# Kernel optimization log

Measured on AMD Instinct MI355X. Metric: run time of the kernel, lower is better.

Reference implementation:

```python
import jax, jax.numpy as jnp
import numpy as np

N_NODES = 50000
N_EDGES = 500000
IN_CH = 128
OUT_CH = 256


def setup_inputs() -> dict:
    key = jax.random.key(0)
    k1, k2, k3, k4, k5 = jax.random.split(key, 5)
    x = jax.random.normal(k1, (N_NODES, IN_CH), dtype=jnp.float32)
    edge_index = jax.random.randint(k2, (2, N_EDGES), 0, N_NODES, dtype=jnp.int64)
    edge_weight = jax.random.normal(k3, (N_EDGES,), dtype=jnp.float32)
    # GCNConv linear weight (xavier-uniform) and bias (zeros in torch init; use randn for generality)
    limit = float(np.sqrt(6.0 / (IN_CH + OUT_CH)))
    W = jax.random.uniform(k4, (IN_CH, OUT_CH), minval=-limit, maxval=limit, dtype=jnp.float32)
    b = jnp.zeros((OUT_CH,), dtype=jnp.float32)
    return {"x": x, "W": W, "b": b, "edge_index": edge_index, "edge_weight": edge_weight}


def reference(x, W, b, edge_index, edge_weight):
    N = x.shape[0]
    # GCN wrapper applies sigmoid to edge weights before GCNConv
    ew = jax.nn.sigmoid(edge_weight)
    # gcn_norm: add self-loops with weight 1
    loop = jnp.arange(N, dtype=edge_index.dtype)
    row = jnp.concatenate([edge_index[0], loop])  # source nodes
    col = jnp.concatenate([edge_index[1], loop])  # target nodes
    w = jnp.concatenate([ew, jnp.ones((N,), dtype=x.dtype)])
    # degree on target index, symmetric normalization
    deg = jax.ops.segment_sum(w, col, num_segments=N)
    dinv = jnp.where(deg > 0, jax.lax.rsqrt(deg), jnp.zeros_like(deg))
    norm = dinv[row] * w * dinv[col]  # [E+N]
    # linear transform first (GCNConv: lin has no bias; bias added after aggregation)
    h = x @ W  # [N, OUT_CH]
    msg = h[row] * norm[:, None]  # gather + scale  [E+N, OUT_CH]
    out = jax.ops.segment_sum(msg, col, num_segments=N) + b
    return out
```

## Files before the change

kernel.cpp:

```cpp
#include <hip/hip_runtime.h>
#include <hip/hip_bf16.h>
#include <math.h>

#define NN 50000
#define NE 500000
#define IC 128
#define OC 256
#define NPAD 50176
#define NB 196
#define NEB 1954
#define CAP 64

typedef short bf16x8 __attribute__((ext_vector_type(8)));
typedef float f32x4 __attribute__((ext_vector_type(4)));

static __device__ inline unsigned short f2b(float f) {
    __hip_bfloat16 h = __float2bfloat16(f);
    return *reinterpret_cast<unsigned short*>(&h);
}
static __device__ inline float b2f(short u) {
    unsigned v = ((unsigned)(unsigned short)u) << 16;
    return __int_as_float(v);
}

__global__ void k_init(unsigned long long* __restrict__ deg64) {
    int i = blockIdx.x * 256 + threadIdx.x;
    deg64[i] = (unsigned long long)(1u << 24);
}

__global__ void k_pass1(const int* __restrict__ row,
                        const int* __restrict__ col,
                        const float* __restrict__ ew,
                        unsigned long long* __restrict__ deg64,
                        int2* __restrict__ epack,
                        const float* __restrict__ x,
                        unsigned short* __restrict__ xb,
                        const float* __restrict__ W,
                        unsigned short* __restrict__ WT) {
    int g = blockIdx.x * 256 + threadIdx.x;
    if (g < NE) {
        int c = col[g];
        float w = 1.0f / (1.0f + expf(-ew[g]));
        unsigned long long pack = (1ull << 32) | (unsigned long long)(unsigned)(w * 16777216.0f);
        unsigned long long old = atomicAdd(&deg64[c], pack);
        int ord = (int)(old >> 32);
        if (ord < CAP) {
            int2 p;
            p.x = row[g];
            p.y = __float_as_int(w);
            epack[(size_t)c * CAP + ord] = p;
        }
    }
    const int NX = NN * (IC / 4);
    for (int i = g; i < NX; i += NEB * 256) {
        float4 v = ((const float4*)x)[i];
        ushort4 o;
        o.x = f2b(v.x); o.y = f2b(v.y); o.z = f2b(v.z); o.w = f2b(v.w);
        ((ushort4*)xb)[i] = o;
    }
    if (g < IC * OC) {
        int k = g >> 8;
        int n = g & 255;
        WT[n * IC + k] = f2b(W[g]);
    }
}

__global__ void k_dinv(const unsigned long long* __restrict__ deg64,
                       float* __restrict__ dinv) {
    int i = blockIdx.x * 256 + threadIdx.x;
    unsigned long long v = deg64[i];
    float deg = (float)(unsigned)v * (1.0f / 16777216.0f);
    dinv[i] = rsqrtf(deg);
}

__global__ __launch_bounds__(256) void k_gather_gemm(
        const unsigned short* __restrict__ xb,
        const unsigned long long* __restrict__ deg64,
        const int2* __restrict__ epack,
        const float* __restrict__ dinv,
        const unsigned short* __restrict__ WT,
        const float* __restrict__ bias,
        float* __restrict__ out) {
    __shared__ __align__(16) unsigned short a[16][136];

    const int base = blockIdx.x * 16;
    const int g = threadIdx.x >> 4;
    const int l16 = threadIdx.x & 15;
    const int n = base + g;
    const bf16x8* xv = (const bf16x8*)xb;

    float di = dinv[n];
    unsigned long long dv = deg64[n];
    int cnt = (int)(dv >> 32);
    if (cnt > CAP) cnt = CAP;

    bf16x8 xs = xv[(size_t)n * 16 + l16];
    float acc[8];
    float s2 = di * di;
    #pragma unroll
    for (int c = 0; c < 8; ++c) acc[c] = b2f(xs[c]) * s2;

    const int2* ep = epack + (size_t)n * CAP;
    int e = 0;
    for (; e + 2 <= cnt; e += 2) {
        int2 p0 = ep[e];
        int2 p1 = ep[e + 1];
        float w0 = __int_as_float(p0.y) * dinv[p0.x] * di;
        float w1 = __int_as_float(p1.y) * dinv[p1.x] * di;
        bf16x8 v0 = xv[(size_t)p0.x * 16 + l16];
        bf16x8 v1 = xv[(size_t)p1.x * 16 + l16];
        #pragma unroll
        for (int c = 0; c < 8; ++c) acc[c] += b2f(v0[c]) * w0;
        #pragma unroll
        for (int c = 0; c < 8; ++c) acc[c] += b2f(v1[c]) * w1;
    }
    if (e < cnt) {
        int2 p = ep[e];
        float w = __int_as_float(p.y) * dinv[p.x] * di;
        bf16x8 v = xv[(size_t)p.x * 16 + l16];
        #pragma unroll
        for (int c = 0; c < 8; ++c) acc[c] += b2f(v[c]) * w;
    }

    bf16x8 o;
    #pragma unroll
    for (int c = 0; c < 8; ++c) o[c] = (short)f2b(acc[c]);
    *(bf16x8*)(&a[g][l16 * 8]) = o;

    __syncthreads();

    const int w = threadIdx.x >> 6;
    const int lane = threadIdx.x & 63;
    const int n0 = w * 64;
    const int lm = lane & 15;
    const int lk = (lane >> 4) * 8;

    f32x4 acc4[4] = {};
    #pragma unroll
    for (int ks = 0; ks < 4; ++ks) {
        const int k0 = ks * 32 + lk;
        bf16x8 wf[4];
        #pragma unroll
        for (int j = 0; j < 4; ++j)
            wf[j] = *(const bf16x8*)(WT + (size_t)(n0 + j * 16 + lm) * IC + k0);
        bf16x8 af = *(const bf16x8*)(&a[lm][k0]);
        #pragma unroll
        for (int j = 0; j < 4; ++j)
            acc4[j] = __builtin_amdgcn_mfma_f32_16x16x32_bf16(wf[j], af, acc4[j], 0, 0, 0);
    }

    const int mcol = lane & 15;
    const int nb4 = (lane >> 4) * 4;
    const int m = base + mcol;
    #pragma unroll
    for (int j = 0; j < 4; ++j) {
        int nn = n0 + j * 16 + nb4;
        float4 bv = *(const float4*)&bias[nn];
        float4 ov;
        ov.x = acc4[j][0] + bv.x;
        ov.y = acc4[j][1] + bv.y;
        ov.z = acc4[j][2] + bv.z;
        ov.w = acc4[j][3] + bv.w;
        *(float4*)(out + (size_t)m * OC + nn) = ov;
    }
}

extern "C" void kernel_launch(void* const* d_in, const int* in_sizes, int n_in,
                              void* d_out, int out_size, void* d_ws, size_t ws_size,
                              hipStream_t stream) {
    const float* x  = (const float*)d_in[0];
    const float* W  = (const float*)d_in[1];
    const float* b  = (const float*)d_in[2];
    const int*   ei = (const int*)d_in[3];
    const float* ew = (const float*)d_in[4];
    const int* row = ei;
    const int* col = ei + NE;
    float* out = (float*)d_out;

    char* w0 = (char*)d_ws;
    unsigned long long* deg64 = (unsigned long long*)w0;  w0 += NPAD * 8;
    float* dinv  = (float*)w0;                   w0 += NPAD * 4;
    int2*  epack = (int2*)w0;                    w0 += (size_t)NN * CAP * 8;
    unsigned short* WT   = (unsigned short*)w0;  w0 += IC * OC * 2;
    unsigned short* xb   = (unsigned short*)w0;

    k_init       <<<NB, 256, 0, stream>>>(deg64);
    k_pass1      <<<NEB, 256, 0, stream>>>(row, col, ew, deg64, epack, x, xb, W, WT);
    k_dinv       <<<NB, 256, 0, stream>>>(deg64, dinv);
    k_gather_gemm<<<NN / 16, 256, 0, stream>>>(xb, deg64, epack, dinv, WT, b, out);
}
```

Baseline: 175.6 us.

## Pack edges into 32-bit words and process 32 nodes per gather-GEMM block

Each edge entry shrinks from 8 to 4 bytes by storing a 16-bit source index with an fp16 sigmoid weight. The gather-GEMM block now handles 32 nodes, with 8 lanes per node each loading two bf16x8 chunks. The next edge pair is prefetched, and each loaded W fragment feeds two MFMA row tiles, halving W loads per node. This lowers edge-list traffic and W reloads, at the cost of reduced edge-weight precision, a 16-bit node-index limit, and a prefetch read past each list that relies on padding.

```diff
diff --git a/kernel.cpp b/kernel.cpp
--- a/kernel.cpp
+++ b/kernel.cpp
@@ -1,5 +1,6 @@
 #include <hip/hip_runtime.h>
 #include <hip/hip_bf16.h>
+#include <hip/hip_fp16.h>
 #include <math.h>
 
 #define NN 50000
@@ -22,6 +23,10 @@
     unsigned v = ((unsigned)(unsigned short)u) << 16;
     return __int_as_float(v);
 }
+static __device__ inline float h2f(unsigned short h) {
+    __half v = __ushort_as_half(h);
+    return __half2float(v);
+}
 
 __global__ void k_init(unsigned long long* __restrict__ deg64) {
     int i = blockIdx.x * 256 + threadIdx.x;
@@ -32,7 +37,7 @@
                         const int* __restrict__ col,
                         const float* __restrict__ ew,
                         unsigned long long* __restrict__ deg64,
-                        int2* __restrict__ epack,
+                        unsigned* __restrict__ epack,
                         const float* __restrict__ x,
                         unsigned short* __restrict__ xb,
                         const float* __restrict__ W,
@@ -45,9 +50,8 @@
         unsigned long long old = atomicAdd(&deg64[c], pack);
         int ord = (int)(old >> 32);
         if (ord < CAP) {
-            int2 p;
-            p.x = row[g];
-            p.y = __float_as_int(w);
+            unsigned short wh = __half_as_ushort(__float2half_rn(w));
+            unsigned p = ((unsigned)wh << 16) | (unsigned)row[g];
             epack[(size_t)c * CAP + ord] = p;
         }
     }
@@ -76,56 +80,70 @@
 __global__ __launch_bounds__(256) void k_gather_gemm(
         const unsigned short* __restrict__ xb,
         const unsigned long long* __restrict__ deg64,
-        const int2* __restrict__ epack,
+        const unsigned* __restrict__ epack,
         const float* __restrict__ dinv,
         const unsigned short* __restrict__ WT,
         const float* __restrict__ bias,
         float* __restrict__ out) {
-    __shared__ __align__(16) unsigned short a[16][136];
-
-    const int base = blockIdx.x * 16;
-    const int g = threadIdx.x >> 4;
-    const int l16 = threadIdx.x & 15;
+    __shared__ __align__(16) unsigned short a[32][136];
+
+    const int base = blockIdx.x * 32;
+    const int g = threadIdx.x >> 3;
+    const int l8 = threadIdx.x & 7;
     const int n = base + g;
     const bf16x8* xv = (const bf16x8*)xb;
 
-    float di = dinv[n];
-    unsigned long long dv = deg64[n];
-    int cnt = (int)(dv >> 32);
-    if (cnt > CAP) cnt = CAP;
-
-    bf16x8 xs = xv[(size_t)n * 16 + l16];
-    float acc[8];
-    float s2 = di * di;
+    float acc[16];
+    if (n < NN) {
+        float di = dinv[n];
+        unsigned long long dv = deg64[n];
+        int cnt = (int)(dv >> 32);
+        if (cnt > CAP) cnt = CAP;
+        float s2 = di * di;
+
+        bf16x8 xs0 = xv[(size_t)n * 16 + l8];
+        bf16x8 xs1 = xv[(size_t)n * 16 + 8 + l8];
+        #pragma unroll
+        for (int c = 0; c < 8; ++c) { acc[c] = b2f(xs0[c]) * s2; acc[8 + c] = b2f(xs1[c]) * s2; }
+
+        const unsigned* ep = epack + (size_t)n * CAP;
+        int e = 0;
+        uint2 pq = *(const uint2*)ep;
+        for (; e + 2 <= cnt; e += 2) {
+            unsigned p0 = pq.x, p1 = pq.y;
+            pq = *(const uint2*)(ep + e + 2);
+            int r0 = (int)(p0 & 0xFFFFu);
+            int r1 = (int)(p1 & 0xFFFFu);
+            float w0 = h2f((unsigned short)(p0 >> 16)) * dinv[r0] * di;
+            float w1 = h2f((unsigned short)(p1 >> 16)) * dinv[r1] * di;
+            bf16x8 v00 = xv[(size_t)r0 * 16 + l8];
+            bf16x8 v01 = xv[(size_t)r0 * 16 + 8 + l8];
+            bf16x8 v10 = xv[(size_t)r1 * 16 + l8];
+            bf16x8 v11 = xv[(size_t)r1 * 16 + 8 + l8];
+            #pragma unroll
+            for (int c = 0; c < 8; ++c) { acc[c] += b2f(v00[c]) * w0; acc[8 + c] += b2f(v01[c]) * w0; }
+            #pragma unroll
+            for (int c = 0; c < 8; ++c) { acc[c] += b2f(v10[c]) * w1; acc[8 + c] += b2f(v11[c]) * w1; }
+        }
+        if (e < cnt) {
+            unsigned p = pq.x;
+            int r = (int)(p & 0xFFFFu);
+            float w = h2f((unsigned short)(p >> 16)) * dinv[r] * di;
+            bf16x8 v0 = xv[(size_t)r * 16 + l8];
+            bf16x8 v1 = xv[(size_t)r * 16 + 8 + l8];
+            #pragma unroll
+            for (int c = 0; c < 8; ++c) { acc[c] += b2f(v0[c]) * w; acc[8 + c] += b2f(v1[c]) * w; }
+        }
+    } else {
+        #pragma unroll
+        for (int c = 0; c < 16; ++c) acc[c] = 0.0f;
+    }
+
+    bf16x8 o0, o1;
     #pragma unroll
-    for (int c = 0; c < 8; ++c) acc[c] = b2f(xs[c]) * s2;
-
-    const int2* ep = epack + (size_t)n * CAP;
-    int e = 0;
-    for (; e + 2 <= cnt; e += 2) {
-        int2 p0 = ep[e];
-        int2 p1 = ep[e + 1];
-        float w0 = __int_as_float(p0.y) * dinv[p0.x] * di;
-        float w1 = __int_as_float(p1.y) * dinv[p1.x] * di;
-        bf16x8 v0 = xv[(size_t)p0.x * 16 + l16];
-        bf16x8 v1 = xv[(size_t)p1.x * 16 + l16];
-        #pragma unroll
-        for (int c = 0; c < 8; ++c) acc[c] += b2f(v0[c]) * w0;
-        #pragma unroll
-        for (int c = 0; c < 8; ++c) acc[c] += b2f(v1[c]) * w1;
-    }
-    if (e < cnt) {
-        int2 p = ep[e];
-        float w = __int_as_float(p.y) * dinv[p.x] * di;
-        bf16x8 v = xv[(size_t)p.x * 16 + l16];
-        #pragma unroll
-        for (int c = 0; c < 8; ++c) acc[c] += b2f(v[c]) * w;
-    }
-
-    bf16x8 o;
-    #pragma unroll
-    for (int c = 0; c < 8; ++c) o[c] = (short)f2b(acc[c]);
-    *(bf16x8*)(&a[g][l16 * 8]) = o;
+    for (int c = 0; c < 8; ++c) { o0[c] = (short)f2b(acc[c]); o1[c] = (short)f2b(acc[8 + c]); }
+    *(bf16x8*)(&a[g][l8 * 8]) = o0;
+    *(bf16x8*)(&a[g][64 + l8 * 8]) = o1;
 
     __syncthreads();
 
@@ -135,33 +153,42 @@
     const int lm = lane & 15;
     const int lk = (lane >> 4) * 8;
 
-    f32x4 acc4[4] = {};
+    f32x4 acc4[2][4] = {};
     #pragma unroll
     for (int ks = 0; ks < 4; ++ks) {
         const int k0 = ks * 32 + lk;
-        bf16x8 wf[4];
+        bf16x8 wf[4], af[2];
         #pragma unroll
         for (int j = 0; j < 4; ++j)
             wf[j] = *(const bf16x8*)(WT + (size_t)(n0 + j * 16 + lm) * IC + k0);
-        bf16x8 af = *(const bf16x8*)(&a[lm][k0]);
-        #pragma unroll
-        for (int j = 0; j < 4; ++j)
-            acc4[j] = __builtin_amdgcn_mfma_f32_16x16x32_bf16(wf[j], af, acc4[j], 0, 0, 0);
+        #pragma unroll
+        for (int i = 0; i < 2; ++i)
+            af[i] = *(const bf16x8*)(&a[i * 16 + lm][k0]);
+        #pragma unroll
+        for (int i = 0; i < 2; ++i)
+            #pragma unroll
+            for (int j = 0; j < 4; ++j)
+                acc4[i][j] = __builtin_amdgcn_mfma_f32_16x16x32_bf16(wf[j], af[i], acc4[i][j], 0, 0, 0);
     }
 
     const int mcol = lane & 15;
     const int nb4 = (lane >> 4) * 4;
-    const int m = base + mcol;
     #pragma unroll
-    for (int j = 0; j < 4; ++j) {
-        int nn = n0 + j * 16 + nb4;
-        float4 bv = *(const float4*)&bias[nn];
-        float4 ov;
-        ov.x = acc4[j][0] + bv.x;
-        ov.y = acc4[j][1] + bv.y;
-        ov.z = acc4[j][2] + bv.z;
-        ov.w = acc4[j][3] + bv.w;
-        *(float4*)(out + (size_t)m * OC + nn) = ov;
+    for (int i = 0; i < 2; ++i) {
+        int m = base + i * 16 + mcol;
+        if (m < NN) {
+            #pragma unroll
+            for (int j = 0; j < 4; ++j) {
+                int nn = n0 + j * 16 + nb4;
+                float4 bv = *(const float4*)&bias[nn];
+                float4 ov;
+                ov.x = acc4[i][j][0] + bv.x;
+                ov.y = acc4[i][j][1] + bv.y;
+                ov.z = acc4[i][j][2] + bv.z;
+                ov.w = acc4[i][j][3] + bv.w;
+                *(float4*)(out + (size_t)m * OC + nn) = ov;
+            }
+        }
     }
 }
 
@@ -180,12 +207,12 @@
     char* w0 = (char*)d_ws;
     unsigned long long* deg64 = (unsigned long long*)w0;  w0 += NPAD * 8;
     float* dinv  = (float*)w0;                   w0 += NPAD * 4;
-    int2*  epack = (int2*)w0;                    w0 += (size_t)NN * CAP * 8;
+    unsigned* epack = (unsigned*)w0;             w0 += ((size_t)NPAD * CAP + 64) * 4;
     unsigned short* WT   = (unsigned short*)w0;  w0 += IC * OC * 2;
     unsigned short* xb   = (unsigned short*)w0;
 
     k_init       <<<NB, 256, 0, stream>>>(deg64);
     k_pass1      <<<NEB, 256, 0, stream>>>(row, col, ew, deg64, epack, x, xb, W, WT);
     k_dinv       <<<NB, 256, 0, stream>>>(deg64, dinv);
-    k_gather_gemm<<<NN / 16, 256, 0, stream>>>(xb, deg64, epack, dinv, WT, b, out);
-}
+    k_gather_gemm<<<(NN + 31) / 32, 256, 0, stream>>>(xb, deg64, epack, dinv, WT, b, out);
+}
```

After: 168.8 us. -3.9%, faster.
